# Performance work log

Hardware: AMD Instinct MI355X
Metric: run time of the kernel (lower is better)

## Reference

```python
import jax, jax.numpy as jnp
import numpy as np

TAU = 1.0
NORMALIZE = True
EPS = 1e-16


def setup_inputs() -> dict:
    key = jax.random.key(0)
    k1, k2 = jax.random.split(key)
    N, D = 8192, 512
    xi = jax.random.normal(k1, (N, D), dtype=jnp.float32)
    xj = jax.random.normal(k2, (N, D), dtype=jnp.float32)
    return {"xi": xi, "xj": xj}


def reference(xi, xj):
    # sim_mat: [N, N] pairwise similarities
    sim_mat = xi @ xj.T
    if NORMALIZE:
        ni = jnp.linalg.norm(xi, axis=1)  # [N]
        nj = jnp.linalg.norm(xj, axis=1)  # [N]
        sim_mat = sim_mat / jnp.clip(ni[:, None] * nj[None, :], EPS)
    sim_mat = jnp.exp(sim_mat / TAU)
    # matched-pair similarity (diagonal-like term), [N]
    if NORMALIZE:
        sim_match = jnp.exp(jnp.sum(xi * xj, axis=-1) / (ni * nj) / TAU)
    else:
        sim_match = jnp.exp(jnp.sum(xi * xj, axis=-1) / TAU)
    sim_match = jnp.concatenate([sim_match, sim_match], axis=0)  # [2N]
    norm_sum = jnp.exp(jnp.ones((xi.shape[0],), dtype=xi.dtype) / TAU)  # [N]
    row_sum = jnp.sum(sim_mat, axis=-1) - norm_sum  # [N]
    # the torch source divides a [2N] vector by [N]; intended NT-Xent tiles the
    # denominator over both symmetric halves (values identical either way)
    row_sum = jnp.concatenate([row_sum, row_sum], axis=0)  # [2N]
    loss = jnp.mean(-jnp.log(sim_match / row_sum))
    return loss
```

## Files before the change

kernel.cpp:

```cpp
#include <hip/hip_runtime.h>
#include <stdint.h>

#define NR 8192
#define DIM 512
#define BM 128
#define BN 128
#define BK 64

typedef __attribute__((ext_vector_type(8))) __bf16 bf16x8;
typedef __attribute__((ext_vector_type(4))) float f32x4;

static __device__ __forceinline__ unsigned short f2bf(float f) {
    union { float f; uint32_t u; } v; v.f = f;
    uint32_t u = v.u;
    u += 0x7FFFu + ((u >> 16) & 1u);
    return (unsigned short)(u >> 16);
}

static __device__ __forceinline__ void gload_lds16(const void* g, void* l) {
    __builtin_amdgcn_global_load_lds(
        (__attribute__((address_space(1))) void*)(void*)g,
        (__attribute__((address_space(3))) void*)l,
        16, 0, 0);
}

__global__ void prep_kernel(const float* __restrict__ xi, const float* __restrict__ xj,
                            unsigned short* __restrict__ xib, unsigned short* __restrict__ xjb,
                            float* __restrict__ inv_ni, float* __restrict__ inv_nj,
                            float* __restrict__ diag, float* __restrict__ rowsum) {
    const int row = blockIdx.x;
    const int t = threadIdx.x;
    const float4 a = ((const float4*)(xi + (size_t)row * DIM))[t];
    const float4 b = ((const float4*)(xj + (size_t)row * DIM))[t];

    float ssi = a.x*a.x + a.y*a.y + a.z*a.z + a.w*a.w;
    float ssj = b.x*b.x + b.y*b.y + b.z*b.z + b.w*b.w;
    float dot = a.x*b.x + a.y*b.y + a.z*b.z + a.w*b.w;

    ushort4 av = { f2bf(a.x), f2bf(a.y), f2bf(a.z), f2bf(a.w) };
    ushort4 bv = { f2bf(b.x), f2bf(b.y), f2bf(b.z), f2bf(b.w) };
    ((ushort4*)(xib + (size_t)row * DIM))[t] = av;
    ((ushort4*)(xjb + (size_t)row * DIM))[t] = bv;

    #pragma unroll
    for (int m = 32; m >= 1; m >>= 1) {
        ssi += __shfl_xor(ssi, m, 64);
        ssj += __shfl_xor(ssj, m, 64);
        dot += __shfl_xor(dot, m, 64);
    }
    __shared__ float red[6];
    const int wave = t >> 6, lane = t & 63;
    if (lane == 0) { red[wave*3+0] = ssi; red[wave*3+1] = ssj; red[wave*3+2] = dot; }
    __syncthreads();
    if (t == 0) {
        float si = red[0] + red[3];
        float sj = red[1] + red[4];
        float d  = red[2] + red[5];
        float ini = rsqrtf(fmaxf(si, 1e-30f));
        float inj = rsqrtf(fmaxf(sj, 1e-30f));
        inv_ni[row] = ini;
        inv_nj[row] = inj;
        diag[row] = d * ini * inj;
        rowsum[row] = 0.0f;
    }
}

__global__ void gemm_rowsum(const unsigned short* __restrict__ A,
                            const unsigned short* __restrict__ B,
                            const float* __restrict__ inv_ni,
                            const float* __restrict__ inv_nj,
                            float* __restrict__ rowsum) {
    __shared__ unsigned short As[BM * BK];
    __shared__ unsigned short Bs[BN * BK];
    const int tid  = threadIdx.x;
    const int row0 = blockIdx.y * BM;
    const int col0 = blockIdx.x * BN;
    const int wid  = tid >> 6;
    const int lane = tid & 63;
    const int wm = wid >> 1, wn = wid & 1;
    const int lr = lane & 15, lk = lane >> 4;
    const int r_l = tid >> 3;
    const int c8  = tid & 7;

    f32x4 acc[4][4] = {};

    for (int k0 = 0; k0 < DIM; k0 += BK) {
        __syncthreads();
        #pragma unroll
        for (int i = 0; i < 4; ++i) {
            const int r = i * 32 + r_l;
            gload_lds16(A + (size_t)(row0 + r) * DIM + k0 + c8 * 8,
                        As + r * BK + c8 * 8);
            gload_lds16(B + (size_t)(col0 + r) * DIM + k0 + c8 * 8,
                        Bs + r * BK + c8 * 8);
        }
        __syncthreads();
        #pragma unroll
        for (int kk = 0; kk < BK; kk += 32) {
            bf16x8 af[4], bg[4];
            #pragma unroll
            for (int m = 0; m < 4; ++m)
                af[m] = *(const bf16x8*)(As + (wm*64 + m*16 + lr) * BK + kk + lk*8);
            #pragma unroll
            for (int n = 0; n < 4; ++n)
                bg[n] = *(const bf16x8*)(Bs + (wn*64 + n*16 + lr) * BK + kk + lk*8);
            #pragma unroll
            for (int m = 0; m < 4; ++m) {
                #pragma unroll
                for (int n = 0; n < 4; ++n)
                    acc[m][n] = __builtin_amdgcn_mfma_f32_16x16x32_bf16(
                        af[m], bg[n], acc[m][n], 0, 0, 0);
            }
        }
    }

    float inj[4];
    #pragma unroll
    for (int n = 0; n < 4; ++n)
        inj[n] = inv_nj[col0 + wn*64 + n*16 + lr];
    float ini[4][4];
    #pragma unroll
    for (int m = 0; m < 4; ++m)
        #pragma unroll
        for (int e = 0; e < 4; ++e)
            ini[m][e] = inv_ni[row0 + wm*64 + m*16 + lk*4 + e];

    #pragma unroll
    for (int m = 0; m < 4; ++m) {
        #pragma unroll
        for (int e = 0; e < 4; ++e) {
            float s = 0.0f;
            const float in_i = ini[m][e];
            #pragma unroll
            for (int n = 0; n < 4; ++n)
                s += __expf(acc[m][n][e] * in_i * inj[n]);
            s += __shfl_xor(s, 1, 64);
            s += __shfl_xor(s, 2, 64);
            s += __shfl_xor(s, 4, 64);
            s += __shfl_xor(s, 8, 64);
            if (lr == 0)
                atomicAdd(&rowsum[row0 + wm*64 + m*16 + lk*4 + e], s);
        }
    }
}

__global__ void finalize(const float* __restrict__ rowsum,
                         const float* __restrict__ diag,
                         float* __restrict__ out) {
    const float E1 = 2.7182818284590452f;
    float acc = 0.0f;
    for (int i = threadIdx.x; i < NR; i += 256)
        acc += __logf(rowsum[i] - E1) - diag[i];
    #pragma unroll
    for (int m = 32; m >= 1; m >>= 1)
        acc += __shfl_xor(acc, m, 64);
    __shared__ float red[4];
    const int wave = threadIdx.x >> 6, lane = threadIdx.x & 63;
    if (lane == 0) red[wave] = acc;
    __syncthreads();
    if (threadIdx.x == 0)
        out[0] = (red[0] + red[1] + red[2] + red[3]) * (1.0f / NR);
}

extern "C" void kernel_launch(void* const* d_in, const int* in_sizes, int n_in,
                              void* d_out, int out_size, void* d_ws, size_t ws_size,
                              hipStream_t stream) {
    const float* xi = (const float*)d_in[0];
    const float* xj = (const float*)d_in[1];

    char* ws = (char*)d_ws;
    unsigned short* xib = (unsigned short*)ws;
    unsigned short* xjb = xib + (size_t)NR * DIM;
    float* inv_ni = (float*)(xjb + (size_t)NR * DIM);
    float* inv_nj = inv_ni + NR;
    float* diag   = inv_nj + NR;
    float* rowsum = diag + NR;

    prep_kernel<<<NR, 128, 0, stream>>>(xi, xj, xib, xjb, inv_ni, inv_nj, diag, rowsum);
    dim3 grid(NR / BN, NR / BM);
    gemm_rowsum<<<grid, 256, 0, stream>>>(xib, xjb, inv_ni, inv_nj, rowsum);
    finalize<<<1, 256, 0, stream>>>(rowsum, diag, (float*)d_out);
}
```

Measured before the change: 138.2 us.

## Use 256x256 tiles with triple-buffered async LDS pipeline and swizzled layout

```diff
diff --git a/kernel.cpp b/kernel.cpp
--- a/kernel.cpp
+++ b/kernel.cpp
@@ -3,18 +3,20 @@
 
 #define NR 8192
 #define DIM 512
-#define BM 128
-#define BN 128
-#define BK 64
-
+#define BM 256
+#define BN 256
+#define BK 32
+#define NT (DIM / BK)
+
+typedef unsigned short u16;
 typedef __attribute__((ext_vector_type(8))) __bf16 bf16x8;
 typedef __attribute__((ext_vector_type(4))) float f32x4;
 
-static __device__ __forceinline__ unsigned short f2bf(float f) {
+static __device__ __forceinline__ u16 f2bf(float f) {
     union { float f; uint32_t u; } v; v.f = f;
     uint32_t u = v.u;
     u += 0x7FFFu + ((u >> 16) & 1u);
-    return (unsigned short)(u >> 16);
+    return (u16)(u >> 16);
 }
 
 static __device__ __forceinline__ void gload_lds16(const void* g, void* l) {
@@ -25,7 +27,7 @@
 }
 
 __global__ void prep_kernel(const float* __restrict__ xi, const float* __restrict__ xj,
-                            unsigned short* __restrict__ xib, unsigned short* __restrict__ xjb,
+                            u16* __restrict__ xib, u16* __restrict__ xjb,
                             float* __restrict__ inv_ni, float* __restrict__ inv_nj,
                             float* __restrict__ diag, float* __restrict__ rowsum) {
     const int row = blockIdx.x;
@@ -65,72 +67,113 @@
     }
 }
 
-__global__ void gemm_rowsum(const unsigned short* __restrict__ A,
-                            const unsigned short* __restrict__ B,
-                            const float* __restrict__ inv_ni,
-                            const float* __restrict__ inv_nj,
-                            float* __restrict__ rowsum) {
-    __shared__ unsigned short As[BM * BK];
-    __shared__ unsigned short Bs[BN * BK];
-    const int tid  = threadIdx.x;
-    const int row0 = blockIdx.y * BM;
-    const int col0 = blockIdx.x * BN;
-    const int wid  = tid >> 6;
+__global__ __launch_bounds__(512, 2)
+void gemm_rowsum(const u16* __restrict__ A, const u16* __restrict__ B,
+                 const float* __restrict__ inv_ni, const float* __restrict__ inv_nj,
+                 float* __restrict__ rowsum) {
+    __shared__ u16 lds[3][2][BM * BK];
+
+    const int tid = threadIdx.x;
+    const int orig = blockIdx.x;
+    const int swz = (orig & 7) * 128 + (orig >> 3);
+    const int by = swz >> 5, bx = swz & 31;
+    const int row0 = by * BM, col0 = bx * BN;
+
+    const int r_st = tid >> 2;
+    const int lc   = (tid & 3) ^ ((r_st >> 1) & 3);
+    const int stoff = tid * 16;
+    const u16* pA0 = A + (size_t)(row0 + r_st)       * DIM + lc * 8;
+    const u16* pA1 = A + (size_t)(row0 + 128 + r_st) * DIM + lc * 8;
+    const u16* pB0 = B + (size_t)(col0 + r_st)       * DIM + lc * 8;
+    const u16* pB1 = B + (size_t)(col0 + 128 + r_st) * DIM + lc * 8;
+
     const int lane = tid & 63;
-    const int wm = wid >> 1, wn = wid & 1;
     const int lr = lane & 15, lk = lane >> 4;
-    const int r_l = tid >> 3;
-    const int c8  = tid & 7;
-
-    f32x4 acc[4][4] = {};
-
-    for (int k0 = 0; k0 < DIM; k0 += BK) {
-        __syncthreads();
-        #pragma unroll
-        for (int i = 0; i < 4; ++i) {
-            const int r = i * 32 + r_l;
-            gload_lds16(A + (size_t)(row0 + r) * DIM + k0 + c8 * 8,
-                        As + r * BK + c8 * 8);
-            gload_lds16(B + (size_t)(col0 + r) * DIM + k0 + c8 * 8,
-                        Bs + r * BK + c8 * 8);
-        }
-        __syncthreads();
-        #pragma unroll
-        for (int kk = 0; kk < BK; kk += 32) {
-            bf16x8 af[4], bg[4];
-            #pragma unroll
-            for (int m = 0; m < 4; ++m)
-                af[m] = *(const bf16x8*)(As + (wm*64 + m*16 + lr) * BK + kk + lk*8);
-            #pragma unroll
-            for (int n = 0; n < 4; ++n)
-                bg[n] = *(const bf16x8*)(Bs + (wn*64 + n*16 + lr) * BK + kk + lk*8);
-            #pragma unroll
-            for (int m = 0; m < 4; ++m) {
-                #pragma unroll
-                for (int n = 0; n < 4; ++n)
-                    acc[m][n] = __builtin_amdgcn_mfma_f32_16x16x32_bf16(
-                        af[m], bg[n], acc[m][n], 0, 0, 0);
-            }
-        }
-    }
+    const int xsw = lk ^ ((lr >> 1) & 3);
+    const int wid = tid >> 6;
+    const int wm = wid >> 2, wn = wid & 3;
+    const int aoff = (wm * 128 + lr) * BK + xsw * 8;
+    const int boff = (wn * 64  + lr) * BK + xsw * 8;
+
+    f32x4 acc[8][4] = {};
+
+    {
+        char* d0a = (char*)&lds[0][0][0] + stoff;
+        char* d0b = (char*)&lds[0][1][0] + stoff;
+        gload_lds16(pA0 +  0, d0a);
+        gload_lds16(pA1 +  0, d0a + 8192);
+        gload_lds16(pB0 +  0, d0b);
+        gload_lds16(pB1 +  0, d0b + 8192);
+        char* d1a = (char*)&lds[1][0][0] + stoff;
+        char* d1b = (char*)&lds[1][1][0] + stoff;
+        gload_lds16(pA0 + 32, d1a);
+        gload_lds16(pA1 + 32, d1a + 8192);
+        gload_lds16(pB0 + 32, d1b);
+        gload_lds16(pB1 + 32, d1b + 8192);
+    }
+
+    int slot = 0;
+    int s2   = 2;
+    int goff = 64;
+
+#define TILE_BODY(VMSTR, DO_STAGE)                                             \
+  do {                                                                         \
+    asm volatile("s_waitcnt vmcnt(" VMSTR ")\ns_barrier" ::: "memory");        \
+    const u16* As_ = &lds[slot][0][0];                                         \
+    const u16* Bs_ = &lds[slot][1][0];                                         \
+    bf16x8 af[4], bg[4];                                                       \
+    _Pragma("unroll") for (int n = 0; n < 4; ++n)                              \
+      bg[n] = *(const bf16x8*)(Bs_ + boff + n * 512);                          \
+    _Pragma("unroll") for (int m = 0; m < 4; ++m)                              \
+      af[m] = *(const bf16x8*)(As_ + aoff + m * 512);                          \
+    if (DO_STAGE) {                                                            \
+      char* da = (char*)&lds[s2][0][0] + stoff;                                \
+      gload_lds16(pA0 + goff, da);                                             \
+      gload_lds16(pA1 + goff, da + 8192);                                      \
+    }                                                                          \
+    __builtin_amdgcn_s_setprio(1);                                             \
+    _Pragma("unroll") for (int m = 0; m < 4; ++m)                              \
+      _Pragma("unroll") for (int n = 0; n < 4; ++n)                            \
+        acc[m][n] = __builtin_amdgcn_mfma_f32_16x16x32_bf16(                   \
+            af[m], bg[n], acc[m][n], 0, 0, 0);                                 \
+    __builtin_amdgcn_s_setprio(0);                                             \
+    _Pragma("unroll") for (int m = 0; m < 4; ++m)                              \
+      af[m] = *(const bf16x8*)(As_ + aoff + (4 + m) * 512);                    \
+    if (DO_STAGE) {                                                            \
+      char* db = (char*)&lds[s2][1][0] + stoff;                                \
+      gload_lds16(pB0 + goff, db);                                             \
+      gload_lds16(pB1 + goff, db + 8192);                                      \
+      goff += 32;                                                              \
+    }                                                                          \
+    __builtin_amdgcn_s_setprio(1);                                             \
+    _Pragma("unroll") for (int m = 0; m < 4; ++m)                              \
+      _Pragma("unroll") for (int n = 0; n < 4; ++n)                            \
+        acc[4 + m][n] = __builtin_amdgcn_mfma_f32_16x16x32_bf16(               \
+            af[m], bg[n], acc[4 + m][n], 0, 0, 0);                             \
+    __builtin_amdgcn_s_setprio(0);                                             \
+    slot = (slot == 2) ? 0 : slot + 1;                                         \
+    s2   = (s2   == 2) ? 0 : s2   + 1;                                         \
+  } while (0)
+
+    #pragma unroll 1
+    for (int t = 0; t < NT - 2; ++t)
+        TILE_BODY("4", true);
+    TILE_BODY("4", false);
+    TILE_BODY("0", false);
+#undef TILE_BODY
 
     float inj[4];
     #pragma unroll
     for (int n = 0; n < 4; ++n)
-        inj[n] = inv_nj[col0 + wn*64 + n*16 + lr];
-    float ini[4][4];
-    #pragma unroll
-    for (int m = 0; m < 4; ++m)
-        #pragma unroll
-        for (int e = 0; e < 4; ++e)
-            ini[m][e] = inv_ni[row0 + wm*64 + m*16 + lk*4 + e];
-
-    #pragma unroll
-    for (int m = 0; m < 4; ++m) {
+        inj[n] = inv_nj[col0 + wn * 64 + n * 16 + lr];
+
+    #pragma unroll
+    for (int m = 0; m < 8; ++m) {
         #pragma unroll
         for (int e = 0; e < 4; ++e) {
+            const int row = row0 + wm * 128 + m * 16 + lk * 4 + e;
+            const float in_i = inv_ni[row];
             float s = 0.0f;
-            const float in_i = ini[m][e];
             #pragma unroll
             for (int n = 0; n < 4; ++n)
                 s += __expf(acc[m][n][e] * in_i * inj[n]);
@@ -139,7 +182,7 @@
             s += __shfl_xor(s, 4, 64);
             s += __shfl_xor(s, 8, 64);
             if (lr == 0)
-                atomicAdd(&rowsum[row0 + wm*64 + m*16 + lk*4 + e], s);
+                atomicAdd(&rowsum[row], s);
         }
     }
 }
@@ -169,15 +212,14 @@
     const float* xj = (const float*)d_in[1];
 
     char* ws = (char*)d_ws;
-    unsigned short* xib = (unsigned short*)ws;
-    unsigned short* xjb = xib + (size_t)NR * DIM;
+    u16* xib = (u16*)ws;
+    u16* xjb = xib + (size_t)NR * DIM;
     float* inv_ni = (float*)(xjb + (size_t)NR * DIM);
     float* inv_nj = inv_ni + NR;
     float* diag   = inv_nj + NR;
     float* rowsum = diag + NR;
 
     prep_kernel<<<NR, 128, 0, stream>>>(xi, xj, xib, xjb, inv_ni, inv_nj, diag, rowsum);
-    dim3 grid(NR / BN, NR / BM);
-    gemm_rowsum<<<grid, 256, 0, stream>>>(xib, xjb, inv_ni, inv_nj, rowsum);
+    gemm_rowsum<<<(NR / BM) * (NR / BN), 512, 0, stream>>>(xib, xjb, inv_ni, inv_nj, rowsum);
     finalize<<<1, 256, 0, stream>>>(rowsum, diag, (float*)d_out);
 }
```

New measurement: 176.5 us. 27.7% more time.

## Switch similarity GEMM to FP8 scaled MFMA with swizzled LDS and XCD block mapping

Applied to the files above, without the earlier changes.

```diff
diff --git a/kernel.cpp b/kernel.cpp
--- a/kernel.cpp
+++ b/kernel.cpp
@@ -2,20 +2,15 @@
 #include <stdint.h>
 
 #define NR 8192
-#define DIM 512
-#define BM 128
-#define BN 128
-#define BK 64
+#define DIMB 512
+#define BT 128
+#define KT 128
+#define NTILE (DIMB / KT)
+#define SCALE1 0x7F7F7F7F
 
-typedef __attribute__((ext_vector_type(8))) __bf16 bf16x8;
+typedef uint8_t u8;
+typedef __attribute__((ext_vector_type(8))) int i32x8;
 typedef __attribute__((ext_vector_type(4))) float f32x4;
-
-static __device__ __forceinline__ unsigned short f2bf(float f) {
-    union { float f; uint32_t u; } v; v.f = f;
-    uint32_t u = v.u;
-    u += 0x7FFFu + ((u >> 16) & 1u);
-    return (unsigned short)(u >> 16);
-}
 
 static __device__ __forceinline__ void gload_lds16(const void* g, void* l) {
     __builtin_amdgcn_global_load_lds(
@@ -24,23 +19,35 @@
         16, 0, 0);
 }
 
+static __device__ __forceinline__ i32x8 read32(const u8* pLo, const u8* pHi) {
+    int4 lo = *(const int4*)pLo;
+    int4 hi = *(const int4*)pHi;
+    i32x8 v;
+    v[0] = lo.x; v[1] = lo.y; v[2] = lo.z; v[3] = lo.w;
+    v[4] = hi.x; v[5] = hi.y; v[6] = hi.z; v[7] = hi.w;
+    return v;
+}
+
 __global__ void prep_kernel(const float* __restrict__ xi, const float* __restrict__ xj,
-                            unsigned short* __restrict__ xib, unsigned short* __restrict__ xjb,
+                            u8* __restrict__ xib, u8* __restrict__ xjb,
                             float* __restrict__ inv_ni, float* __restrict__ inv_nj,
                             float* __restrict__ diag, float* __restrict__ rowsum) {
     const int row = blockIdx.x;
     const int t = threadIdx.x;
-    const float4 a = ((const float4*)(xi + (size_t)row * DIM))[t];
-    const float4 b = ((const float4*)(xj + (size_t)row * DIM))[t];
+    const float4 a = ((const float4*)(xi + (size_t)row * 512))[t];
+    const float4 b = ((const float4*)(xj + (size_t)row * 512))[t];
 
     float ssi = a.x*a.x + a.y*a.y + a.z*a.z + a.w*a.w;
     float ssj = b.x*b.x + b.y*b.y + b.z*b.z + b.w*b.w;
     float dot = a.x*b.x + a.y*b.y + a.z*b.z + a.w*b.w;
 
-    ushort4 av = { f2bf(a.x), f2bf(a.y), f2bf(a.z), f2bf(a.w) };
-    ushort4 bv = { f2bf(b.x), f2bf(b.y), f2bf(b.z), f2bf(b.w) };
-    ((ushort4*)(xib + (size_t)row * DIM))[t] = av;
-    ((ushort4*)(xjb + (size_t)row * DIM))[t] = bv;
+    int pa = 0, pb = 0;
+    pa = __builtin_amdgcn_cvt_pk_fp8_f32(a.x, a.y, pa, false);
+    pa = __builtin_amdgcn_cvt_pk_fp8_f32(a.z, a.w, pa, true);
+    pb = __builtin_amdgcn_cvt_pk_fp8_f32(b.x, b.y, pb, false);
+    pb = __builtin_amdgcn_cvt_pk_fp8_f32(b.z, b.w, pb, true);
+    ((int*)(xib + (size_t)row * DIMB))[t] = pa;
+    ((int*)(xjb + (size_t)row * DIMB))[t] = pb;
 
     #pragma unroll
     for (int m = 32; m >= 1; m >>= 1) {
@@ -65,72 +72,79 @@
     }
 }
 
-__global__ void gemm_rowsum(const unsigned short* __restrict__ A,
-                            const unsigned short* __restrict__ B,
-                            const float* __restrict__ inv_ni,
-                            const float* __restrict__ inv_nj,
-                            float* __restrict__ rowsum) {
-    __shared__ unsigned short As[BM * BK];
-    __shared__ unsigned short Bs[BN * BK];
-    const int tid  = threadIdx.x;
-    const int row0 = blockIdx.y * BM;
-    const int col0 = blockIdx.x * BN;
-    const int wid  = tid >> 6;
+__global__ __launch_bounds__(256, 3)
+void gemm_rowsum(const u8* __restrict__ A8, const u8* __restrict__ B8,
+                 const float* __restrict__ inv_ni, const float* __restrict__ inv_nj,
+                 float* __restrict__ rowsum) {
+    __shared__ __align__(16) u8 ldsA[BT * KT];
+    __shared__ __align__(16) u8 ldsB[BT * KT];
+
+    const int tid = threadIdx.x;
+    const int orig = blockIdx.x;
+    const int xcd = orig & 7, kk = orig >> 3;
+    const int by = xcd * 8 + (kk & 7);
+    const int bx = kk >> 3;
+    const int row0 = by * BT, col0 = bx * BT;
+
+    const int r0 = tid >> 3;
+    const int lc = (tid & 7) ^ (r0 & 7);
+    const u8* gA = A8 + (size_t)(row0 + r0) * DIMB + lc * 16;
+    const u8* gB = B8 + (size_t)(col0 + r0) * DIMB + lc * 16;
+    u8* const dA = ldsA + tid * 16;
+    u8* const dB = ldsB + tid * 16;
+
     const int lane = tid & 63;
+    const int lr = lane & 15, lk = lane >> 4;
+    const int wid = tid >> 6;
     const int wm = wid >> 1, wn = wid & 1;
-    const int lr = lane & 15, lk = lane >> 4;
-    const int r_l = tid >> 3;
-    const int c8  = tid & 7;
+    const int swz = lr & 7;
+    const int cLo = ((lk * 2) ^ swz) * 16;
+    const int cHi = ((lk * 2 + 1) ^ swz) * 16;
+    const u8* const aLo = ldsA + (wm * 64 + lr) * 128 + cLo;
+    const u8* const aHi = ldsA + (wm * 64 + lr) * 128 + cHi;
+    const u8* const bLo = ldsB + (wn * 64 + lr) * 128 + cLo;
+    const u8* const bHi = ldsB + (wn * 64 + lr) * 128 + cHi;
 
     f32x4 acc[4][4] = {};
 
-    for (int k0 = 0; k0 < DIM; k0 += BK) {
-        __syncthreads();
+    #pragma unroll
+    for (int t = 0; t < NTILE; ++t) {
+        if (t) __syncthreads();
         #pragma unroll
         for (int i = 0; i < 4; ++i) {
-            const int r = i * 32 + r_l;
-            gload_lds16(A + (size_t)(row0 + r) * DIM + k0 + c8 * 8,
-                        As + r * BK + c8 * 8);
-            gload_lds16(B + (size_t)(col0 + r) * DIM + k0 + c8 * 8,
-                        Bs + r * BK + c8 * 8);
+            gload_lds16(gA + t * KT + i * 32 * DIMB, dA + i * 4096);
+            gload_lds16(gB + t * KT + i * 32 * DIMB, dB + i * 4096);
         }
+        asm volatile("s_waitcnt vmcnt(0)" ::: "memory");
         __syncthreads();
+
+        i32x8 af[4];
         #pragma unroll
-        for (int kk = 0; kk < BK; kk += 32) {
-            bf16x8 af[4], bg[4];
+        for (int m = 0; m < 4; ++m)
+            af[m] = read32(aLo + m * 2048, aHi + m * 2048);
+        #pragma unroll
+        for (int n = 0; n < 4; ++n) {
+            const i32x8 bg = read32(bLo + n * 2048, bHi + n * 2048);
             #pragma unroll
             for (int m = 0; m < 4; ++m)
-                af[m] = *(const bf16x8*)(As + (wm*64 + m*16 + lr) * BK + kk + lk*8);
-            #pragma unroll
-            for (int n = 0; n < 4; ++n)
-                bg[n] = *(const bf16x8*)(Bs + (wn*64 + n*16 + lr) * BK + kk + lk*8);
-            #pragma unroll
-            for (int m = 0; m < 4; ++m) {
-                #pragma unroll
-                for (int n = 0; n < 4; ++n)
-                    acc[m][n] = __builtin_amdgcn_mfma_f32_16x16x32_bf16(
-                        af[m], bg[n], acc[m][n], 0, 0, 0);
-            }
+                acc[m][n] = __builtin_amdgcn_mfma_scale_f32_16x16x128_f8f6f4(
+                    af[m], bg, acc[m][n], 0 , 0 ,
+                    0, SCALE1, 0, SCALE1);
         }
     }
 
     float inj[4];
     #pragma unroll
     for (int n = 0; n < 4; ++n)
-        inj[n] = inv_nj[col0 + wn*64 + n*16 + lr];
-    float ini[4][4];
-    #pragma unroll
-    for (int m = 0; m < 4; ++m)
-        #pragma unroll
-        for (int e = 0; e < 4; ++e)
-            ini[m][e] = inv_ni[row0 + wm*64 + m*16 + lk*4 + e];
+        inj[n] = inv_nj[col0 + wn * 64 + n * 16 + lr];
 
     #pragma unroll
     for (int m = 0; m < 4; ++m) {
         #pragma unroll
         for (int e = 0; e < 4; ++e) {
+            const int row = row0 + wm * 64 + m * 16 + lk * 4 + e;
+            const float in_i = inv_ni[row];
             float s = 0.0f;
-            const float in_i = ini[m][e];
             #pragma unroll
             for (int n = 0; n < 4; ++n)
                 s += __expf(acc[m][n][e] * in_i * inj[n]);
@@ -139,7 +153,7 @@
             s += __shfl_xor(s, 4, 64);
             s += __shfl_xor(s, 8, 64);
             if (lr == 0)
-                atomicAdd(&rowsum[row0 + wm*64 + m*16 + lk*4 + e], s);
+                atomicAdd(&rowsum[row], s);
         }
     }
 }
@@ -169,15 +183,14 @@
     const float* xj = (const float*)d_in[1];
 
     char* ws = (char*)d_ws;
-    unsigned short* xib = (unsigned short*)ws;
-    unsigned short* xjb = xib + (size_t)NR * DIM;
-    float* inv_ni = (float*)(xjb + (size_t)NR * DIM);
+    u8* xib = (u8*)ws;
+    u8* xjb = xib + (size_t)NR * DIMB;
+    float* inv_ni = (float*)(xjb + (size_t)NR * DIMB);
     float* inv_nj = inv_ni + NR;
     float* diag   = inv_nj + NR;
     float* rowsum = diag + NR;
 
     prep_kernel<<<NR, 128, 0, stream>>>(xi, xj, xib, xjb, inv_ni, inv_nj, diag, rowsum);
-    dim3 grid(NR / BN, NR / BM);
-    gemm_rowsum<<<grid, 256, 0, stream>>>(xib, xjb, inv_ni, inv_nj, rowsum);
+    gemm_rowsum<<<(NR / BT) * (NR / BT), 256, 0, stream>>>(xib, xjb, inv_ni, inv_nj, rowsum);
     finalize<<<1, 256, 0, stream>>>(rowsum, diag, (float*)d_out);
 }
```

New measurement: 289.9 us. +109.8%, slower.

## Swizzle LDS layout, remap blocks per XCD, and add launch bounds in GEMM

Applied to the files above, without the earlier changes.

```diff
diff --git a/kernel.cpp b/kernel.cpp
--- a/kernel.cpp
+++ b/kernel.cpp
@@ -3,18 +3,19 @@
 
 #define NR 8192
 #define DIM 512
-#define BM 128
-#define BN 128
+#define BT 128
 #define BK 64
+#define NT (DIM / BK)
 
+typedef unsigned short u16;
 typedef __attribute__((ext_vector_type(8))) __bf16 bf16x8;
 typedef __attribute__((ext_vector_type(4))) float f32x4;
 
-static __device__ __forceinline__ unsigned short f2bf(float f) {
+static __device__ __forceinline__ u16 f2bf(float f) {
     union { float f; uint32_t u; } v; v.f = f;
     uint32_t u = v.u;
     u += 0x7FFFu + ((u >> 16) & 1u);
-    return (unsigned short)(u >> 16);
+    return (u16)(u >> 16);
 }
 
 static __device__ __forceinline__ void gload_lds16(const void* g, void* l) {
@@ -25,7 +26,7 @@
 }
 
 __global__ void prep_kernel(const float* __restrict__ xi, const float* __restrict__ xj,
-                            unsigned short* __restrict__ xib, unsigned short* __restrict__ xjb,
+                            u16* __restrict__ xib, u16* __restrict__ xjb,
                             float* __restrict__ inv_ni, float* __restrict__ inv_nj,
                             float* __restrict__ diag, float* __restrict__ rowsum) {
     const int row = blockIdx.x;
@@ -65,72 +66,80 @@
     }
 }
 
-__global__ void gemm_rowsum(const unsigned short* __restrict__ A,
-                            const unsigned short* __restrict__ B,
-                            const float* __restrict__ inv_ni,
-                            const float* __restrict__ inv_nj,
-                            float* __restrict__ rowsum) {
-    __shared__ unsigned short As[BM * BK];
-    __shared__ unsigned short Bs[BN * BK];
-    const int tid  = threadIdx.x;
-    const int row0 = blockIdx.y * BM;
-    const int col0 = blockIdx.x * BN;
-    const int wid  = tid >> 6;
+__global__ __launch_bounds__(256, 4)
+void gemm_rowsum(const u16* __restrict__ A, const u16* __restrict__ B,
+                 const float* __restrict__ inv_ni, const float* __restrict__ inv_nj,
+                 float* __restrict__ rowsum) {
+    __shared__ __align__(16) u16 ldsA[BT * BK];
+    __shared__ __align__(16) u16 ldsB[BT * BK];
+
+    const int tid = threadIdx.x;
+    const int orig = blockIdx.x;
+    const int xcd = orig & 7, kidx = orig >> 3;
+    const int by = xcd * 8 + (kidx & 7);
+    const int bx = kidx >> 3;
+    const int row0 = by * BT, col0 = bx * BT;
+
+    const int st_row = tid >> 3;
+    const int st_lc  = (tid & 7) ^ (st_row & 7);
+    const u16* gA = A + (size_t)(row0 + st_row) * DIM + st_lc * 8;
+    const u16* gB = B + (size_t)(col0 + st_row) * DIM + st_lc * 8;
+    char* const dA = (char*)ldsA + tid * 16;
+    char* const dB = (char*)ldsB + tid * 16;
+
     const int lane = tid & 63;
+    const int lr = lane & 15, lk = lane >> 4;
+    const int wid = tid >> 6;
     const int wm = wid >> 1, wn = wid & 1;
-    const int lr = lane & 15, lk = lane >> 4;
-    const int r_l = tid >> 3;
-    const int c8  = tid & 7;
+    const int sw = lr & 7;
+    const int c0 = (lk ^ sw) * 16;
+    const int c1 = ((4 + lk) ^ sw) * 16;
+    const char* const aR = (const char*)ldsA + (wm * 64 + lr) * 128;
+    const char* const bR = (const char*)ldsB + (wn * 64 + lr) * 128;
 
     f32x4 acc[4][4] = {};
 
-    for (int k0 = 0; k0 < DIM; k0 += BK) {
-        __syncthreads();
+    #pragma unroll 1
+    for (int t = 0; t < NT; ++t) {
+        if (t) __syncthreads();
         #pragma unroll
         for (int i = 0; i < 4; ++i) {
-            const int r = i * 32 + r_l;
-            gload_lds16(A + (size_t)(row0 + r) * DIM + k0 + c8 * 8,
-                        As + r * BK + c8 * 8);
-            gload_lds16(B + (size_t)(col0 + r) * DIM + k0 + c8 * 8,
-                        Bs + r * BK + c8 * 8);
+            gload_lds16(gA + t * BK + i * 32 * DIM, dA + i * 4096);
+            gload_lds16(gB + t * BK + i * 32 * DIM, dB + i * 4096);
         }
         __syncthreads();
+
         #pragma unroll
-        for (int kk = 0; kk < BK; kk += 32) {
+        for (int kk = 0; kk < 2; ++kk) {
+            const int cb = kk ? c1 : c0;
             bf16x8 af[4], bg[4];
             #pragma unroll
             for (int m = 0; m < 4; ++m)
-                af[m] = *(const bf16x8*)(As + (wm*64 + m*16 + lr) * BK + kk + lk*8);
+                af[m] = *(const bf16x8*)(aR + m * 2048 + cb);
             #pragma unroll
             for (int n = 0; n < 4; ++n)
-                bg[n] = *(const bf16x8*)(Bs + (wn*64 + n*16 + lr) * BK + kk + lk*8);
+                bg[n] = *(const bf16x8*)(bR + n * 2048 + cb);
             #pragma unroll
-            for (int m = 0; m < 4; ++m) {
+            for (int m = 0; m < 4; ++m)
                 #pragma unroll
                 for (int n = 0; n < 4; ++n)
                     acc[m][n] = __builtin_amdgcn_mfma_f32_16x16x32_bf16(
                         af[m], bg[n], acc[m][n], 0, 0, 0);
-            }
         }
     }
 
     float inj[4];
     #pragma unroll
     for (int n = 0; n < 4; ++n)
-        inj[n] = inv_nj[col0 + wn*64 + n*16 + lr];
-    float ini[4][4];
-    #pragma unroll
-    for (int m = 0; m < 4; ++m)
-        #pragma unroll
-        for (int e = 0; e < 4; ++e)
-            ini[m][e] = inv_ni[row0 + wm*64 + m*16 + lk*4 + e];
+        inj[n] = inv_nj[col0 + wn * 64 + n * 16 + lr];
 
     #pragma unroll
     for (int m = 0; m < 4; ++m) {
         #pragma unroll
         for (int e = 0; e < 4; ++e) {
+            const int row = row0 + wm * 64 + m * 16 + lk * 4 + e;
+            const float in_i = inv_ni[row];
             float s = 0.0f;
-            const float in_i = ini[m][e];
             #pragma unroll
             for (int n = 0; n < 4; ++n)
                 s += __expf(acc[m][n][e] * in_i * inj[n]);
@@ -139,7 +148,7 @@
             s += __shfl_xor(s, 4, 64);
             s += __shfl_xor(s, 8, 64);
             if (lr == 0)
-                atomicAdd(&rowsum[row0 + wm*64 + m*16 + lk*4 + e], s);
+                atomicAdd(&rowsum[row], s);
         }
     }
 }
@@ -169,15 +178,14 @@
     const float* xj = (const float*)d_in[1];
 
     char* ws = (char*)d_ws;
-    unsigned short* xib = (unsigned short*)ws;
-    unsigned short* xjb = xib + (size_t)NR * DIM;
+    u16* xib = (u16*)ws;
+    u16* xjb = xib + (size_t)NR * DIM;
     float* inv_ni = (float*)(xjb + (size_t)NR * DIM);
     float* inv_nj = inv_ni + NR;
     float* diag   = inv_nj + NR;
     float* rowsum = diag + NR;
 
     prep_kernel<<<NR, 128, 0, stream>>>(xi, xj, xib, xjb, inv_ni, inv_nj, diag, rowsum);
-    dim3 grid(NR / BN, NR / BM);
-    gemm_rowsum<<<grid, 256, 0, stream>>>(xib, xjb, inv_ni, inv_nj, rowsum);
+    gemm_rowsum<<<(NR / BT) * (NR / BT), 256, 0, stream>>>(xib, xjb, inv_ni, inv_nj, rowsum);
     finalize<<<1, 256, 0, stream>>>(rowsum, diag, (float*)d_out);
 }
```

Result: faster. 113.5 us (-17.8%).
